# Optimization experiments

Measured on AMD Instinct MI355X. Metric: run time of the kernel, lower is better.

## Reference

```python
import jax, jax.numpy as jnp
import numpy as np

B, H, W, N, DX, DZ = 4, 64, 64, 4096, 2, 128
INIT_LS = 0.1


def setup_inputs() -> dict:
    key = jax.random.key(0)
    k1, k2, k3, k4 = jax.random.split(key, 4)
    xc_off_grid = jax.random.uniform(k1, (B, N, DX), dtype=jnp.float32)
    # regular grid coordinates in [0, 1]^2, broadcast over batch
    gy, gx = jnp.meshgrid(jnp.linspace(0.0, 1.0, H), jnp.linspace(0.0, 1.0, W), indexing="ij")
    xc_on_grid = jnp.broadcast_to(jnp.stack([gy, gx], axis=-1)[None], (B, H, W, DX)).astype(jnp.float32)
    zc_off_grid = jax.random.normal(k2, (B, N, DZ), dtype=jnp.float32)
    zc_on_grid = jax.random.normal(k3, (B, H, W, DZ), dtype=jnp.float32)
    # lengthscale_param = log(exp(init_lengthscale) - 1)  (inverse softplus)
    lengthscale_param = jnp.log(jnp.expm1(jnp.full((DX,), INIT_LS, dtype=jnp.float32)))
    return {
        "xc_off_grid": xc_off_grid,
        "xc_on_grid": xc_on_grid,
        "zc_off_grid": zc_off_grid,
        "zc_on_grid": zc_on_grid,
        "lengthscale_param": lengthscale_param,
        "ignore_on_grid": 0,
    }


def reference(xc_off_grid, xc_on_grid, zc_off_grid, zc_on_grid, lengthscale_param, ignore_on_grid):
    b = xc_on_grid.shape[0]
    grid_shape = xc_on_grid.shape[1:-1]
    dz = zc_off_grid.shape[-1]
    xg = xc_on_grid.reshape(b, -1, xc_on_grid.shape[-1])  # [b, m, dx]
    lengthscale = 1e-05 + jax.nn.softplus(lengthscale_param)  # [dx]
    # squared scaled distances: [b, m, n]
    diff = (xg[:, :, None, :] - xc_off_grid[:, None, :, :]) / lengthscale
    weights = jnp.exp(-0.5 * jnp.sum(diff * diff, axis=-1))  # [b, m, n]
    zc = jnp.einsum("bmn,bnd->bmd", weights, zc_off_grid)  # [b, m, dz]
    if not ignore_on_grid:
        zc = zc + zc_on_grid.reshape(b, -1, dz)
    return zc.reshape((b,) + grid_shape + (dz,))
```

## Files before the change

### kernel.cpp

```cpp
#include <hip/hip_runtime.h>

#define HH 64
#define WW 64
#define NN 4096
#define DZc 128
#define KS 8
#define BK 64
#define NKT (NN / KS / BK)
#define CELLS 2097152
#define ZT_BYTES (4ull * 128 * 4096 * 2ull)
#define WS_NEED (ZT_BYTES + 8ull * CELLS * 2ull)

typedef __fp16 v2fp16 __attribute__((ext_vector_type(2)));
typedef _Float16 v4h __attribute__((ext_vector_type(4)));
typedef _Float16 v8h __attribute__((ext_vector_type(8)));
typedef float v16f __attribute__((ext_vector_type(16)));

__device__ __forceinline__ unsigned pk16(float lo, float hi){
  union { v2fp16 h; unsigned u; } c;
  c.h = __builtin_amdgcn_cvt_pkrtz(lo, hi);
  return c.u;
}
__device__ __forceinline__ float fexp2(float x){ return __builtin_amdgcn_exp2f(x); }

__global__ __launch_bounds__(256, 8)
void init_out_kernel(const float4* __restrict__ zc_on,
                     const int* __restrict__ ignore,
                     float4* __restrict__ out){
  int i = blockIdx.x * blockDim.x + threadIdx.x;
  float4 v = zc_on[i];
  if (ignore[0]) { v.x = 0.f; v.y = 0.f; v.z = 0.f; v.w = 0.f; }
  out[i] = v;
}

__global__ __launch_bounds__(256, 4)
void prepack_kernel(const float* __restrict__ zc_off, _Float16* __restrict__ zf){
  __shared__ unsigned tt[128 * 36];
  const int bidx = blockIdx.x;
  const int b  = bidx >> 6;
  const int nt = bidx & 63;
  const int n0 = nt * 64;
  const int t  = threadIdx.x;

  const int np = t >> 3;
  const int d0 = (t & 7) * 16;
  const float* r0 = zc_off + ((size_t)(b * NN + n0 + 2 * np)) * DZc + d0;
  float4 a[4], c[4];
  #pragma unroll
  for (int i = 0; i < 4; ++i){
    a[i] = *(const float4*)&r0[4 * i];
    c[i] = *(const float4*)&r0[DZc + 4 * i];
  }
  const float* af = (const float*)a;
  const float* cf = (const float*)c;
  #pragma unroll
  for (int j = 0; j < 16; ++j)
    tt[(d0 + j) * 36 + np] = pk16(af[j], cf[j]);

  __syncthreads();

  const int dblk = t >> 6;
  const int q    = t & 63;
  const int d    = dblk * 32 + (q >> 1);
  const int lh   = q & 1;
  _Float16* ob = zf + ((size_t)(b * 64 + nt)) * 8192;
  #pragma unroll
  for (int p = 0; p < 4; ++p){
    uint4 w = *(const uint4*)&tt[d * 36 + p * 8 + lh * 4];
    *(uint4*)&ob[(size_t)((p * 4 + dblk) * 64 + q) * 8] = w;
  }
}

__global__ __launch_bounds__(256, 8)
void reduce_kernel(const v8h* __restrict__ part,
                   const float4* __restrict__ zc_on,
                   const int* __restrict__ ignore,
                   float4* __restrict__ out){
  int i = blockIdx.x * blockDim.x + threadIdx.x;
  float4 s0 = zc_on[2 * i];
  float4 s1 = zc_on[2 * i + 1];
  if (ignore[0]) {
    s0.x = s0.y = s0.z = s0.w = 0.f;
    s1.x = s1.y = s1.z = s1.w = 0.f;
  }
  #pragma unroll
  for (int ks = 0; ks < KS; ++ks){
    v8h p = part[(size_t)ks * (CELLS / 8) + i];
    s0.x += (float)p[0]; s0.y += (float)p[1]; s0.z += (float)p[2]; s0.w += (float)p[3];
    s1.x += (float)p[4]; s1.y += (float)p[5]; s1.z += (float)p[6]; s1.w += (float)p[7];
  }
  out[2 * i]     = s0;
  out[2 * i + 1] = s1;
}

__global__ __launch_bounds__(256, 4)
void setconv_gemm_pre(const float* __restrict__ xc_off,
                      const float* __restrict__ xc_on,
                      const _Float16* __restrict__ zpack,
                      const float* __restrict__ lsp,
                      _Float16* __restrict__ part)
{
  __shared__ unsigned short gt[2][24][72];

  const int tid = threadIdx.x;
  const int rawb = blockIdx.x;
  const int lb = (rawb & 7) * 128 + (rawb >> 3);
  const int ks = lb >> 7;
  const int bm = lb & 127;
  const int b  = bm >> 5;
  const int mt = bm & 31;
  const int iy0 = (mt >> 3) * 16;
  const int ix0 = (mt & 7) * 8;

  const float lsy = 1e-5f + log1pf(expf(lsp[0]));
  const float lsx = 1e-5f + log1pf(expf(lsp[1]));
  const float LOG2E = 1.44269504088896340736f;
  const float ay = -0.5f * LOG2E / (lsy * lsy);
  const float ax = -0.5f * LOG2E / (lsx * lsx);

  const int gp = tid & 31;
  const int gr = tid >> 5;
  float gc[3], ga[3];
  #pragma unroll
  for (int i = 0; i < 3; ++i){
    int row = gr + 8 * i;
    if (row < 16){ gc[i] = xc_on[((b * HH + iy0 + row) * WW) * 2];        ga[i] = ay; }
    else         { gc[i] = xc_on[(b * HH * WW + ix0 + row - 16) * 2 + 1]; ga[i] = ax; }
  }

  const int lane = tid & 63;
  const int wv  = tid >> 6;
  const int mq  = wv >> 1;
  const int dh  = wv & 1;
  const int l31 = lane & 31;
  const int lh  = lane >> 5;
  const int gxr = 16 + (l31 & 7);
  const int gyr = mq * 8 + (l31 >> 3);
  const int dblk0 = dh * 2;
  const int q = l31 * 2 + lh;

  v16f acc[2][2];
  #pragma unroll
  for (int m = 0; m < 2; ++m)
    #pragma unroll
    for (int d = 0; d < 2; ++d)
      #pragma unroll
      for (int r = 0; r < 16; ++r)
        acc[m][d][r] = 0.f;

  const float* xb = xc_off + (size_t)b * NN * 2;
  const _Float16* zb0 = zpack + ((size_t)(b * 64 + ks * NKT)) * 8192
                              + (size_t)(dblk0 * 64 + q) * 8;

  {
    float4 xq = *(const float4*)&xb[(size_t)(ks * (NN / KS) + 2 * gp) * 2];
    unsigned* gw = (unsigned*)&gt[0][0][0];
    #pragma unroll
    for (int i = 0; i < 3; ++i){
      int row = gr + 8 * i;
      float s0 = (row < 16) ? xq.x : xq.y;
      float s1 = (row < 16) ? xq.z : xq.w;
      float d0 = gc[i] - s0, d1 = gc[i] - s1;
      gw[row * 36 + gp] = pk16(fexp2(ga[i] * d0 * d0), fexp2(ga[i] * d1 * d1));
    }
  }
  __syncthreads();

  #pragma unroll 1
  for (int kt = 0; kt < NKT; ++kt){
    const int buf  = kt & 1;
    const int nbuf = buf ^ 1;
    const bool have_next = (kt + 1 < NKT);

    float4 xq_n = (float4){0.f, 0.f, 0.f, 0.f};
    if (have_next)
      xq_n = *(const float4*)&xb[(size_t)(ks * (NN / KS) + (kt + 1) * BK + 2 * gp) * 2];

    const _Float16* zk = zb0 + (size_t)kt * 8192;

    __builtin_amdgcn_s_setprio(1);
    #pragma unroll
    for (int kstep = 0; kstep < 4; ++kstep){
      const int k0 = kstep * 16 + lh * 8;
      const v8h xu = *(const v8h*)&gt[buf][gxr][k0];
      const v8h bf0 = *(const v8h*)&zk[kstep * 2048];
      const v8h bf1 = *(const v8h*)&zk[kstep * 2048 + 512];
      #pragma unroll
      for (int mtl = 0; mtl < 2; ++mtl){
        const v8h yu = *(const v8h*)&gt[buf][gyr + mtl * 4][k0];
        v8h av = yu * xu;
        acc[mtl][0] = __builtin_amdgcn_mfma_f32_32x32x16_f16(av, bf0, acc[mtl][0], 0, 0, 0);
        acc[mtl][1] = __builtin_amdgcn_mfma_f32_32x32x16_f16(av, bf1, acc[mtl][1], 0, 0, 0);
      }
    }
    __builtin_amdgcn_s_setprio(0);

    if (have_next){
      unsigned* gw = (unsigned*)&gt[nbuf][0][0];
      #pragma unroll
      for (int i = 0; i < 3; ++i){
        int row = gr + 8 * i;
        float s0 = (row < 16) ? xq_n.x : xq_n.y;
        float s1 = (row < 16) ? xq_n.z : xq_n.w;
        float d0 = gc[i] - s0, d1 = gc[i] - s1;
        gw[row * 36 + gp] = pk16(fexp2(ga[i] * d0 * d0), fexp2(ga[i] * d1 * d1));
      }
    }
    __syncthreads();
  }

  _Float16* pw = part + (size_t)ks * CELLS;
  #pragma unroll
  for (int mtl = 0; mtl < 2; ++mtl)
    #pragma unroll
    for (int dtl = 0; dtl < 2; ++dtl){
      const int d = dh * 64 + dtl * 32 + l31;
      #pragma unroll
      for (int reg = 0; reg < 16; ++reg){
        const int row = (reg & 3) + 8 * (reg >> 2) + 4 * lh;
        const int m = mq * 64 + mtl * 32 + row;
        const int iy = iy0 + (m >> 3);
        const int ix = ix0 + (m & 7);
        pw[((b * HH + iy) * WW + ix) * DZc + d] = (_Float16)acc[mtl][dtl][reg];
      }
    }
}

__global__ __launch_bounds__(512, 4)
void setconv_gemm_fb(const float* __restrict__ xc_off,
                     const float* __restrict__ xc_on,
                     const float* __restrict__ zc_off,
                     const float* __restrict__ lsp,
                     float* __restrict__ out)
{
  __shared__ unsigned short zt[2][128][68];
  __shared__ unsigned short gt[2][40][72];

  const int tid = threadIdx.x;
  const int bid = blockIdx.x;
  const int ks  = bid >> 6;
  const int bm  = bid & 63;
  const int b   = bm >> 4;
  const int mt  = bm & 15;
  const int iy0 = (mt >> 3) * 32;
  const int ix0 = (mt & 7) * 8;
  const int nbase = ks * (NN / KS);

  const float lsy = 1e-5f + log1pf(expf(lsp[0]));
  const float lsx = 1e-5f + log1pf(expf(lsp[1]));
  const float LOG2E = 1.44269504088896340736f;
  const float ay = -0.5f * LOG2E / (lsy * lsy);
  const float ax = -0.5f * LOG2E / (lsx * lsx);

  const int gp = tid & 31;
  const int gr = tid >> 5;
  float gc[3], ga[3];
  #pragma unroll
  for (int i = 0; i < 3; ++i){
    int row = gr + 16 * i;
    if (row < 32)      { gc[i] = xc_on[((b * HH + iy0 + row) * WW) * 2];        ga[i] = ay; }
    else if (row < 40) { gc[i] = xc_on[(b * HH * WW + ix0 + row - 32) * 2 + 1]; ga[i] = ax; }
    else               { gc[i] = 0.f; ga[i] = 0.f; }
  }

  const int zd = tid & 127;
  const int zq = tid >> 7;

  const int lane = tid & 63;
  const int wv  = tid >> 6;
  const int mq  = wv >> 1;
  const int dh  = wv & 1;
  const int l31 = lane & 31;
  const int lh  = lane >> 5;
  const int gxr = 32 + (l31 & 7);
  const int gyr = mq * 8 + (l31 >> 3);
  const int dbase = dh * 64;

  v16f acc[2][2];
  #pragma unroll
  for (int m = 0; m < 2; ++m)
    #pragma unroll
    for (int d = 0; d < 2; ++d)
      #pragma unroll
      for (int r = 0; r < 16; ++r)
        acc[m][d][r] = 0.f;

  const float* xb = xc_off + (size_t)b * NN * 2;
  const float* zb = zc_off + (size_t)b * NN * DZc;

  {
    const int n0 = nbase;
    float4 xq = *(const float4*)&xb[(size_t)(n0 + 2 * gp) * 2];
    unsigned* gw = (unsigned*)&gt[0][0][0];
    #pragma unroll
    for (int i = 0; i < 3; ++i){
      int row = gr + 16 * i;
      if (row < 40){
        float s0 = (row < 32) ? xq.x : xq.y;
        float s1 = (row < 32) ? xq.z : xq.w;
        float d0 = gc[i] - s0, d1 = gc[i] - s1;
        gw[row * 36 + gp] = pk16(fexp2(ga[i] * d0 * d0), fexp2(ga[i] * d1 * d1));
      }
    }
    float zv[16];
    #pragma unroll
    for (int i = 0; i < 16; ++i)
      zv[i] = zb[(size_t)(n0 + zq * 16 + i) * DZc + zd];
    #pragma unroll
    for (int j = 0; j < 4; ++j){
      union { unsigned u[2]; double dd; } w;
      w.u[0] = pk16(zv[4 * j],     zv[4 * j + 1]);
      w.u[1] = pk16(zv[4 * j + 2], zv[4 * j + 3]);
      *(double*)&zt[0][zd][zq * 16 + 4 * j] = w.dd;
    }
  }
  __syncthreads();

  #pragma unroll 1
  for (int kt = 0; kt < NKT; ++kt){
    const int buf  = kt & 1;
    const int nbuf = buf ^ 1;
    const bool have_next = (kt + 1 < NKT);
    const int n1 = nbase + (kt + 1) * BK;

    float zv[16];
    float4 xq_n = (float4){0.f, 0.f, 0.f, 0.f};
    if (have_next){
      #pragma unroll
      for (int i = 0; i < 16; ++i)
        zv[i] = zb[(size_t)(n1 + zq * 16 + i) * DZc + zd];
      xq_n = *(const float4*)&xb[(size_t)(n1 + 2 * gp) * 2];
    }

    #pragma unroll
    for (int kstep = 0; kstep < 4; ++kstep){
      const int k0 = kstep * 16 + lh * 8;
      const v8h xu = *(const v8h*)&gt[buf][gxr][k0];
      v8h bfr[2];
      #pragma unroll
      for (int dtl = 0; dtl < 2; ++dtl){
        union { v4h h[2]; v8h v; } zu;
        zu.h[0] = *(const v4h*)&zt[buf][dbase + dtl * 32 + l31][k0];
        zu.h[1] = *(const v4h*)&zt[buf][dbase + dtl * 32 + l31][k0 + 4];
        bfr[dtl] = zu.v;
      }
      #pragma unroll
      for (int mtl = 0; mtl < 2; ++mtl){
        const v8h yu = *(const v8h*)&gt[buf][gyr + mtl * 4][k0];
        v8h av = yu * xu;
        #pragma unroll
        for (int dtl = 0; dtl < 2; ++dtl)
          acc[mtl][dtl] = __builtin_amdgcn_mfma_f32_32x32x16_f16(av, bfr[dtl], acc[mtl][dtl], 0, 0, 0);
      }
    }

    if (have_next){
      #pragma unroll
      for (int j = 0; j < 4; ++j){
        union { unsigned u[2]; double dd; } w;
        w.u[0] = pk16(zv[4 * j],     zv[4 * j + 1]);
        w.u[1] = pk16(zv[4 * j + 2], zv[4 * j + 3]);
        *(double*)&zt[nbuf][zd][zq * 16 + 4 * j] = w.dd;
      }
      unsigned* gw = (unsigned*)&gt[nbuf][0][0];
      #pragma unroll
      for (int i = 0; i < 3; ++i){
        int row = gr + 16 * i;
        if (row < 40){
          float s0 = (row < 32) ? xq_n.x : xq_n.y;
          float s1 = (row < 32) ? xq_n.z : xq_n.w;
          float d0 = gc[i] - s0, d1 = gc[i] - s1;
          gw[row * 36 + gp] = pk16(fexp2(ga[i] * d0 * d0), fexp2(ga[i] * d1 * d1));
        }
      }
    }
    __syncthreads();
  }

  #pragma unroll
  for (int mtl = 0; mtl < 2; ++mtl)
    #pragma unroll
    for (int dtl = 0; dtl < 2; ++dtl){
      const int d = dbase + dtl * 32 + l31;
      #pragma unroll
      for (int reg = 0; reg < 16; ++reg){
        const int row = (reg & 3) + 8 * (reg >> 2) + 4 * lh;
        const int m = mq * 64 + mtl * 32 + row;
        const int iy = iy0 + (m >> 3);
        const int ix = ix0 + (m & 7);
        unsafeAtomicAdd(&out[((b * HH + iy) * WW + ix) * DZc + d], acc[mtl][dtl][reg]);
      }
    }
}

extern "C" void kernel_launch(void* const* d_in, const int* in_sizes, int n_in,
                              void* d_out, int out_size, void* d_ws, size_t ws_size,
                              hipStream_t stream){
  const float* xc_off = (const float*)d_in[0];
  const float* xc_on  = (const float*)d_in[1];
  const float* zc_off = (const float*)d_in[2];
  const float* zc_on  = (const float*)d_in[3];
  const float* lsp    = (const float*)d_in[4];
  const int*   ign    = (const int*)d_in[5];
  float* out = (float*)d_out;

  if (ws_size >= WS_NEED){
    _Float16* zpack = (_Float16*)d_ws;
    _Float16* part  = (_Float16*)((char*)d_ws + ZT_BYTES);
    prepack_kernel<<<4 * 64, 256, 0, stream>>>(zc_off, zpack);
    setconv_gemm_pre<<<KS * 128, 256, 0, stream>>>(xc_off, xc_on, zpack, lsp, part);
    reduce_kernel<<<CELLS / 8 / 256, 256, 0, stream>>>((const v8h*)part, (const float4*)zc_on, ign, (float4*)out);
  } else {
    init_out_kernel<<<CELLS / 4 / 256, 256, 0, stream>>>((const float4*)zc_on, ign, (float4*)out);
    setconv_gemm_fb<<<KS * 64, 512, 0, stream>>>(xc_off, xc_on, zc_off, lsp, out);
  }
}
```

Baseline: 107.0 us.

## Stage packed Z tile through shared memory and halve the K-split count

The prepack kernel now writes Z as a simple transposed [b][d][n] fp16 layout. The GEMM kernel stages each 128x64 Z tile into a double-buffered LDS array instead of reading MFMA B fragments straight from global memory. The global loads for the next tile are issued before the MFMAs, which overlaps their latency with compute. KS drops from 8 to 4, which halves the partial-sum buffer and the reduce work but doubles each block's K loop and gives fewer blocks. The extra LDS traffic and lower occupancy may offset some of the gain.

```diff
diff --git a/kernel.cpp b/kernel.cpp
--- a/kernel.cpp
+++ b/kernel.cpp
@@ -4,17 +4,18 @@
 #define WW 64
 #define NN 4096
 #define DZc 128
-#define KS 8
+#define KS 4
 #define BK 64
 #define NKT (NN / KS / BK)
 #define CELLS 2097152
 #define ZT_BYTES (4ull * 128 * 4096 * 2ull)
-#define WS_NEED (ZT_BYTES + 8ull * CELLS * 2ull)
+#define WS_NEED (ZT_BYTES + (unsigned long long)KS * CELLS * 2ull)
 
 typedef __fp16 v2fp16 __attribute__((ext_vector_type(2)));
 typedef _Float16 v4h __attribute__((ext_vector_type(4)));
 typedef _Float16 v8h __attribute__((ext_vector_type(8)));
 typedef float v16f __attribute__((ext_vector_type(16)));
+typedef double v2d __attribute__((ext_vector_type(2)));
 
 __device__ __forceinline__ unsigned pk16(float lo, float hi){
   union { v2fp16 h; unsigned u; } c;
@@ -34,12 +35,11 @@
 }
 
 __global__ __launch_bounds__(256, 4)
-void prepack_kernel(const float* __restrict__ zc_off, _Float16* __restrict__ zf){
-  __shared__ unsigned tt[128 * 36];
+void prepack_kernel(const float* __restrict__ zc_off, _Float16* __restrict__ zt_g){
+  __shared__ unsigned tt[128 * 34];
   const int bidx = blockIdx.x;
   const int b  = bidx >> 6;
-  const int nt = bidx & 63;
-  const int n0 = nt * 64;
+  const int n0 = (bidx & 63) * 64;
   const int t  = threadIdx.x;
 
   const int np = t >> 3;
@@ -55,19 +55,21 @@
   const float* cf = (const float*)c;
   #pragma unroll
   for (int j = 0; j < 16; ++j)
-    tt[(d0 + j) * 36 + np] = pk16(af[j], cf[j]);
+    tt[(d0 + j) * 34 + np] = pk16(af[j], cf[j]);
 
   __syncthreads();
 
-  const int dblk = t >> 6;
-  const int q    = t & 63;
-  const int d    = dblk * 32 + (q >> 1);
-  const int lh   = q & 1;
-  _Float16* ob = zf + ((size_t)(b * 64 + nt)) * 8192;
-  #pragma unroll
-  for (int p = 0; p < 4; ++p){
-    uint4 w = *(const uint4*)&tt[d * 36 + p * 8 + lh * 4];
-    *(uint4*)&ob[(size_t)((p * 4 + dblk) * 64 + q) * 8] = w;
+  const int d  = t >> 1;
+  const int nh = t & 1;
+  const unsigned* rr = tt + d * 34 + nh * 16;
+  _Float16* w = zt_g + ((size_t)(b * DZc + d)) * NN + n0 + nh * 32;
+  double v[8];
+  #pragma unroll
+  for (int j = 0; j < 8; ++j) v[j] = *(const double*)&rr[2 * j];
+  #pragma unroll
+  for (int j = 0; j < 4; ++j){
+    v2d s; s[0] = v[2 * j]; s[1] = v[2 * j + 1];
+    *(v2d*)&w[8 * j] = s;
   }
 }
 
@@ -100,17 +102,19 @@
                       const float* __restrict__ lsp,
                       _Float16* __restrict__ part)
 {
+  __shared__ unsigned short zt[2][128][68];
   __shared__ unsigned short gt[2][24][72];
 
   const int tid = threadIdx.x;
   const int rawb = blockIdx.x;
-  const int lb = (rawb & 7) * 128 + (rawb >> 3);
+  const int lb = (rawb & 7) * 64 + (rawb >> 3);
   const int ks = lb >> 7;
   const int bm = lb & 127;
   const int b  = bm >> 5;
   const int mt = bm & 31;
   const int iy0 = (mt >> 3) * 16;
   const int ix0 = (mt & 7) * 8;
+  const int nbase = ks * (NN / KS);
 
   const float lsy = 1e-5f + log1pf(expf(lsp[0]));
   const float lsx = 1e-5f + log1pf(expf(lsp[1]));
@@ -127,6 +131,10 @@
     if (row < 16){ gc[i] = xc_on[((b * HH + iy0 + row) * WW) * 2];        ga[i] = ay; }
     else         { gc[i] = xc_on[(b * HH * WW + ix0 + row - 16) * 2 + 1]; ga[i] = ax; }
   }
+
+  const int zd  = (tid & 63) | (((tid >> 6) & 1) << 6);
+  const int zkh = tid >> 7;
+  const _Float16* ztg = zpack + ((size_t)(b * DZc + zd)) * NN + nbase + zkh * 32;
 
   const int lane = tid & 63;
   const int wv  = tid >> 6;
@@ -136,8 +144,7 @@
   const int lh  = lane >> 5;
   const int gxr = 16 + (l31 & 7);
   const int gyr = mq * 8 + (l31 >> 3);
-  const int dblk0 = dh * 2;
-  const int q = l31 * 2 + lh;
+  const int dbase = dh * 64;
 
   v16f acc[2][2];
   #pragma unroll
@@ -149,11 +156,9 @@
         acc[m][d][r] = 0.f;
 
   const float* xb = xc_off + (size_t)b * NN * 2;
-  const _Float16* zb0 = zpack + ((size_t)(b * 64 + ks * NKT)) * 8192
-                              + (size_t)(dblk0 * 64 + q) * 8;
 
   {
-    float4 xq = *(const float4*)&xb[(size_t)(ks * (NN / KS) + 2 * gp) * 2];
+    float4 xq = *(const float4*)&xb[(size_t)(nbase + 2 * gp) * 2];
     unsigned* gw = (unsigned*)&gt[0][0][0];
     #pragma unroll
     for (int i = 0; i < 3; ++i){
@@ -163,6 +168,13 @@
       float d0 = gc[i] - s0, d1 = gc[i] - s1;
       gw[row * 36 + gp] = pk16(fexp2(ga[i] * d0 * d0), fexp2(ga[i] * d1 * d1));
     }
+    #pragma unroll
+    for (int i = 0; i < 4; ++i){
+      union { v8h v; double d[2]; } u;
+      u.v = *(const v8h*)&ztg[8 * i];
+      *(double*)&zt[0][zd][zkh * 32 + 8 * i]     = u.d[0];
+      *(double*)&zt[0][zd][zkh * 32 + 8 * i + 4] = u.d[1];
+    }
   }
   __syncthreads();
 
@@ -172,30 +184,47 @@
     const int nbuf = buf ^ 1;
     const bool have_next = (kt + 1 < NKT);
 
+    v8h zrn[4];
     float4 xq_n = (float4){0.f, 0.f, 0.f, 0.f};
-    if (have_next)
-      xq_n = *(const float4*)&xb[(size_t)(ks * (NN / KS) + (kt + 1) * BK + 2 * gp) * 2];
-
-    const _Float16* zk = zb0 + (size_t)kt * 8192;
+    if (have_next){
+      #pragma unroll
+      for (int i = 0; i < 4; ++i)
+        zrn[i] = *(const v8h*)&ztg[(kt + 1) * BK + 8 * i];
+      xq_n = *(const float4*)&xb[(size_t)(nbase + (kt + 1) * BK + 2 * gp) * 2];
+    }
 
     __builtin_amdgcn_s_setprio(1);
     #pragma unroll
     for (int kstep = 0; kstep < 4; ++kstep){
       const int k0 = kstep * 16 + lh * 8;
       const v8h xu = *(const v8h*)&gt[buf][gxr][k0];
-      const v8h bf0 = *(const v8h*)&zk[kstep * 2048];
-      const v8h bf1 = *(const v8h*)&zk[kstep * 2048 + 512];
+      v8h bfr[2];
+      #pragma unroll
+      for (int dtl = 0; dtl < 2; ++dtl){
+        union { v4h h[2]; v8h v; } zu;
+        zu.h[0] = *(const v4h*)&zt[buf][dbase + dtl * 32 + l31][k0];
+        zu.h[1] = *(const v4h*)&zt[buf][dbase + dtl * 32 + l31][k0 + 4];
+        bfr[dtl] = zu.v;
+      }
       #pragma unroll
       for (int mtl = 0; mtl < 2; ++mtl){
         const v8h yu = *(const v8h*)&gt[buf][gyr + mtl * 4][k0];
         v8h av = yu * xu;
-        acc[mtl][0] = __builtin_amdgcn_mfma_f32_32x32x16_f16(av, bf0, acc[mtl][0], 0, 0, 0);
-        acc[mtl][1] = __builtin_amdgcn_mfma_f32_32x32x16_f16(av, bf1, acc[mtl][1], 0, 0, 0);
+        #pragma unroll
+        for (int dtl = 0; dtl < 2; ++dtl)
+          acc[mtl][dtl] = __builtin_amdgcn_mfma_f32_32x32x16_f16(av, bfr[dtl], acc[mtl][dtl], 0, 0, 0);
       }
     }
     __builtin_amdgcn_s_setprio(0);
 
     if (have_next){
+      #pragma unroll
+      for (int i = 0; i < 4; ++i){
+        union { v8h v; double d[2]; } u;
+        u.v = zrn[i];
+        *(double*)&zt[nbuf][zd][zkh * 32 + 8 * i]     = u.d[0];
+        *(double*)&zt[nbuf][zd][zkh * 32 + 8 * i + 4] = u.d[1];
+      }
       unsigned* gw = (unsigned*)&gt[nbuf][0][0];
       #pragma unroll
       for (int i = 0; i < 3; ++i){
@@ -214,7 +243,7 @@
   for (int mtl = 0; mtl < 2; ++mtl)
     #pragma unroll
     for (int dtl = 0; dtl < 2; ++dtl){
-      const int d = dh * 64 + dtl * 32 + l31;
+      const int d = dbase + dtl * 32 + l31;
       #pragma unroll
       for (int reg = 0; reg < 16; ++reg){
         const int row = (reg & 3) + 8 * (reg >> 2) + 4 * lh;
```

Result: no change. 107.6 us (+0.6%).
